# Kernel optimization log

Measured on AMD Instinct MI355X. Metric: run time of the kernel, lower is better.

Reference implementation:

```python
import jax, jax.numpy as jnp
import numpy as np
from itertools import combinations

S = 7                       # number of species (H,C,N,O,S,F,Cl)
RCR, RCA = 5.2, 3.5         # radial / angular cutoffs (Angstrom)
ETA_R, ETA_A, ZETA = 19.7, 12.5, 14.1
SHF_R = jnp.asarray(0.8 + 0.275 * np.arange(16), jnp.float32)        # 16 radial shifts
SHF_A = jnp.asarray(0.8 + 0.3375 * np.arange(8), jnp.float32)        # 8 angular radial shifts
SHF_Z = jnp.asarray((np.arange(4) + 0.5) * np.pi / 4, jnp.float32)   # 4 angle shifts
NPAIR = S * (S + 1) // 2    # 28 unordered species pairs
_t = np.zeros((S, S), np.int32); _c = 0
for _a in range(S):
    for _b in range(_a, S):
        _t[_a, _b] = _t[_b, _a] = _c; _c += 1
TRIU = jnp.asarray(_t)
AEV_DIM = S * 16 + NPAIR * 32   # 1008
M, H1, H2, H3 = 8, 256, 192, 160  # ensemble size and MLP widths


def _fc(d, rc):
    # torchani cutoff_cosine, masked for safety beyond rc
    return jnp.where(d < rc, 0.5 * jnp.cos(jnp.pi * d / rc) + 0.5, 0.0)


def compute_aev(sp, coords, atom_index12, triplet_index):
    # sp:[N] int, coords:[N,3], atom_index12:[2,P] half neighbor list,
    # triplet_index:[3,T] = (center, neighbor_j, neighbor_k)
    N = sp.shape[0]
    i, j = atom_index12[0], atom_index12[1]
    dvec = coords[j] - coords[i]
    dist = jnp.sqrt((dvec * dvec).sum(-1))
    fc = _fc(dist, RCR)
    rterm = 0.25 * jnp.exp(-ETA_R * (dist[:, None] - SHF_R) ** 2) * fc[:, None]  # [P,16]
    rad = jnp.zeros((N * S, 16), rterm.dtype)
    rad = rad.at[i * S + sp[j]].add(rterm).at[j * S + sp[i]].add(rterm)
    rad = rad.reshape(N, S * 16)

    c, a, b = triplet_index[0], triplet_index[1], triplet_index[2]
    v1 = coords[a] - coords[c]
    v2 = coords[b] - coords[c]
    d1 = jnp.sqrt((v1 * v1).sum(-1))
    d2 = jnp.sqrt((v2 * v2).sum(-1))
    cosang = 0.95 * (v1 * v2).sum(-1) / (d1 * d2)   # 0.95 numerical-safety factor as in torchani
    ang = jnp.arccos(cosang)
    fcj = _fc(d1, RCA) * _fc(d2, RCA)
    f1 = ((1.0 + jnp.cos(ang[:, None] - SHF_Z)) / 2.0) ** ZETA              # [T,4]
    f2 = jnp.exp(-ETA_A * ((d1 + d2)[:, None] / 2.0 - SHF_A) ** 2)          # [T,8]
    aterm = 2.0 * (f2[:, :, None] * f1[:, None, :]).reshape(-1, 32) * fcj[:, None]  # [T,32]
    pidx = TRIU[sp[a], sp[b]]
    angv = jnp.zeros((N * NPAIR, 32), aterm.dtype).at[c * NPAIR + pidx].add(aterm)
    return jnp.concatenate([rad, angv.reshape(N, NPAIR * 32)], axis=-1)     # [N,1008]


def _energy_and_force(species, coordinates, atom_index12, triplet_index, sgp,
                      W1, b1, W2, b2, W3, b3, W4, b4, sae):
    sp = species[0]
    sgpv = sgp[0]

    def total(coords):
        aev = compute_aev(sp, coords[0], atom_index12, triplet_index)       # [N,1008]
        h = jax.nn.celu(jnp.einsum('na,msab->msnb', aev, W1) + b1[:, :, None, :], alpha=0.1)
        h = jax.nn.celu(jnp.einsum('msnb,msbc->msnc', h, W2) + b2[:, :, None, :], alpha=0.1)
        h = jax.nn.celu(jnp.einsum('msnc,mscd->msnd', h, W3) + b3[:, :, None, :], alpha=0.1)
        e = jnp.einsum('msnd,msd->msn', h, W4) + b4[:, :, None]             # [M,S,N]
        onehot = (sgpv[None, :] == jnp.arange(S)[:, None]).astype(e.dtype)  # ghosts (-1) -> all-zero
        atomic = (e * onehot[None]).sum(1).mean(0)                           # [N] ensemble mean
        atomic = atomic + jnp.where(sgpv >= 0, sae[jnp.clip(sgpv, 0)], 0.0)  # energy shifter SAEs
        return atomic.sum()

    E = total(coordinates)
    force = -jax.grad(total)(coordinates)   # autograd force as in forward_total
    return E[None], force


def setup_inputs() -> dict:
    key = jax.random.key(0)
    n = 14; N = n ** 3   # 2744 atoms on a jittered cubic lattice (2.5 A spacing)
    ar = np.arange(n)
    gx, gy, gz = np.meshgrid(ar, ar, ar, indexing='ij')
    pos = np.stack([gx, gy, gz], -1).reshape(-1, 3)
    lid = lambda p: (p[:, 0] * n + p[:, 1]) * n + p[:, 2]
    # half neighbor list: all lattice offsets with |r| <= 5.2/2.5 lattice units
    half = [(1,0,0),(0,1,0),(0,0,1),(1,1,0),(1,-1,0),(1,0,1),(1,0,-1),(0,1,1),(0,1,-1),
            (1,1,1),(1,1,-1),(1,-1,1),(1,-1,-1),(2,0,0),(0,2,0),(0,0,2)]
    ei, ej = [], []
    for off in half:
        q = pos + np.array(off)
        m = ((q >= 0) & (q < n)).all(1)
        ei.append(lid(pos[m])); ej.append(lid(q[m]))
    atom_index12 = np.stack([np.concatenate(ei), np.concatenate(ej)]).astype(np.int32)
    # angular triplets: pairs of unit-offset neighbors (within Rca=3.5 A) per center
    unit = [(1,0,0),(-1,0,0),(0,1,0),(0,-1,0),(0,0,1),(0,0,-1)]
    nb = np.full((N, 6), -1, np.int64)
    for t, off in enumerate(unit):
        q = pos + np.array(off)
        m = ((q >= 0) & (q < n)).all(1)
        nb[lid(pos[m]), t] = lid(q[m])
    tc, tj, tk = [], [], []
    for a_, b_ in combinations(range(6), 2):
        m = (nb[:, a_] >= 0) & (nb[:, b_] >= 0)
        tc.append(np.nonzero(m)[0]); tj.append(nb[m, a_]); tk.append(nb[m, b_])
    triplet_index = np.stack([np.concatenate(tc), np.concatenate(tj), np.concatenate(tk)]).astype(np.int32)
    rng = np.random.default_rng(0)
    species = rng.integers(0, S, (1, N)).astype(np.int32)
    nghost = 250
    sgp = species.copy(); sgp[0, N - nghost:] = -1   # ghost atoms padded with -1
    coords = (pos.astype(np.float32) * 2.5 + 0.15 * rng.standard_normal((N, 3)).astype(np.float32))[None]
    ks = jax.random.split(key, 9)
    D = AEV_DIM
    W1 = jax.random.normal(ks[0], (M, S, D, H1), jnp.float32) * (D ** -0.5)
    b1 = 0.01 * jax.random.normal(ks[1], (M, S, H1), jnp.float32)
    W2 = jax.random.normal(ks[2], (M, S, H1, H2), jnp.float32) * (H1 ** -0.5)
    b2 = 0.01 * jax.random.normal(ks[3], (M, S, H2), jnp.float32)
    W3 = jax.random.normal(ks[4], (M, S, H2, H3), jnp.float32) * (H2 ** -0.5)
    b3 = 0.01 * jax.random.normal(ks[5], (M, S, H3), jnp.float32)
    W4 = jax.random.normal(ks[6], (M, S, H3), jnp.float32) * (H3 ** -0.5)
    b4 = 0.01 * jax.random.normal(ks[7], (M, S), jnp.float32)
    sae = jax.random.normal(ks[8], (S,), jnp.float32)
    return {
        'species': jnp.asarray(species), 'coordinates': jnp.asarray(coords),
        'atom_index12': jnp.asarray(atom_index12), 'triplet_index': jnp.asarray(triplet_index),
        'species_ghost_as_padding': jnp.asarray(sgp),
        'W1': W1, 'b1': b1, 'W2': W2, 'b2': b2, 'W3': W3, 'b3': b3, 'W4': W4, 'b4': b4, 'sae': sae,
    }


def reference(species, coordinates, atom_index12, triplet_index, species_ghost_as_padding,
              W1, b1, W2, b2, W3, b3, W4, b4, sae):
    return _energy_and_force(species, coordinates, atom_index12, triplet_index,
                             species_ghost_as_padding, W1, b1, W2, b2, W3, b3, W4, b4, sae)
```

## Files before the change

kernel.cpp:

```cpp
#include <hip/hip_runtime.h>
#include <math.h>

constexpr int SPEC = 7;
constexpr int DAEV = 1008;
constexpr int RADN = 112;
constexpr int H1W = 256, H2W = 192, H3W = 160;
constexpr int MENS = 8;
constexpr float ALPHA = 0.1f;
constexpr float RCR_ = 5.2f, RCA_ = 3.5f;
constexpr float ETAR = 19.7f, ETAA = 12.5f, ZETA_ = 14.1f;
constexpr float PIF = 3.14159265358979323846f;

enum { MODE_FWD = 0, MODE_BWD = 1, MODE_PLAIN = 2 };

typedef _Float16 f16x8 __attribute__((ext_vector_type(8)));
typedef float f32x4 __attribute__((ext_vector_type(4)));

__device__ inline f32x4 mfma16(f16x8 a, f16x8 b, f32x4 c) {
    return __builtin_amdgcn_mfma_f32_16x16x32_f16(a, b, c, 0, 0, 0);
}

__device__ inline void cvt_hilo(const float* xv, f16x8& h, f16x8& l) {
    #pragma unroll
    for (int e = 0; e < 8; ++e) {
        _Float16 hh = (_Float16)xv[e];
        h[e] = hh;
        l[e] = (_Float16)(xv[e] - (float)hh);
    }
}

__global__ __launch_bounds__(256) void build_lists_k(
    const int* __restrict__ sgp, int* __restrict__ counts,
    int* __restrict__ lists, int N)
{
    int n = blockIdx.x * blockDim.x + threadIdx.x;
    if (n >= N) return;
    int g = sgp[n];
    if (g >= 0) {
        int p = atomicAdd(&counts[g], 1);
        lists[g * N + p] = n;
    }
}

__global__ __launch_bounds__(256) void radial_fwd_k(
    const int* __restrict__ ai12, const int* __restrict__ spec,
    const float* __restrict__ coord, float* __restrict__ aev, int P)
{
    int p = blockIdx.x * blockDim.x + threadIdx.x;
    if (p >= P) return;
    int i = ai12[p], j = ai12[P + p];
    float dx = coord[3 * j + 0] - coord[3 * i + 0];
    float dy = coord[3 * j + 1] - coord[3 * i + 1];
    float dz = coord[3 * j + 2] - coord[3 * i + 2];
    float d = sqrtf(dx * dx + dy * dy + dz * dz);
    float fc = (d < RCR_) ? (0.5f * cosf(PIF * d / RCR_) + 0.5f) : 0.f;
    int spi = spec[i], spj = spec[j];
    float* bi = aev + (size_t)i * DAEV + spj * 16;
    float* bj = aev + (size_t)j * DAEV + spi * 16;
    #pragma unroll
    for (int k = 0; k < 16; ++k) {
        float sh = 0.8f + 0.275f * k;
        float t = d - sh;
        float v = 0.25f * expf(-ETAR * t * t) * fc;
        atomicAdd(bi + k, v);
        atomicAdd(bj + k, v);
    }
}

__global__ __launch_bounds__(256) void angular_fwd_k(
    const int* __restrict__ tri, const int* __restrict__ spec,
    const float* __restrict__ coord, float* __restrict__ aev, int T)
{
    int t = blockIdx.x * blockDim.x + threadIdx.x;
    if (t >= T) return;
    int c = tri[t], a = tri[T + t], b = tri[2 * T + t];
    float cx = coord[3 * c], cy = coord[3 * c + 1], cz = coord[3 * c + 2];
    float v1x = coord[3 * a] - cx, v1y = coord[3 * a + 1] - cy, v1z = coord[3 * a + 2] - cz;
    float v2x = coord[3 * b] - cx, v2y = coord[3 * b + 1] - cy, v2z = coord[3 * b + 2] - cz;
    float d1 = sqrtf(v1x * v1x + v1y * v1y + v1z * v1z);
    float d2 = sqrtf(v2x * v2x + v2y * v2y + v2z * v2z);
    float u = v1x * v2x + v1y * v2y + v1z * v2z;
    float ca = 0.95f * u / (d1 * d2);
    float sa = sqrtf(fmaxf(1.f - ca * ca, 0.f));
    float fc1 = (d1 < RCA_) ? (0.5f * cosf(PIF * d1 / RCA_) + 0.5f) : 0.f;
    float fc2 = (d2 < RCA_) ? (0.5f * cosf(PIF * d2 / RCA_) + 0.5f) : 0.f;
    float fcj = fc1 * fc2;
    float savg = 0.5f * (d1 + d2);
    int s1 = spec[a], s2 = spec[b];
    int lo = min(s1, s2), hi = max(s1, s2);
    int pidx = lo * SPEC - (lo * (lo - 1)) / 2 + (hi - lo);
    float* ob = aev + (size_t)c * DAEV + RADN + pidx * 32;
    const float CZ[4] = {0.92387953f, 0.38268343f, -0.38268343f, -0.92387953f};
    const float SZ[4] = {0.38268343f, 0.92387953f, 0.92387953f, 0.38268343f};
    float f1[4];
    #pragma unroll
    for (int zz = 0; zz < 4; ++zz) {
        float cd = ca * CZ[zz] + sa * SZ[zz];
        float base = fmaxf(0.5f * (1.f + cd), 0.f);
        f1[zz] = powf(base, ZETA_);
    }
    #pragma unroll
    for (int q = 0; q < 8; ++q) {
        float sh = 0.8f + 0.3375f * q;
        float tq = savg - sh;
        float f2 = expf(-ETAA * tq * tq);
        float b2 = 2.f * f2 * fcj;
        #pragma unroll
        for (int zz = 0; zz < 4; ++zz)
            atomicAdd(ob + q * 4 + zz, b2 * f1[zz]);
    }
}

template<int MODE, bool BT, bool MCONCAT>
__global__ __launch_bounds__(256) void mgemm_k(
    const float* __restrict__ A, const float* __restrict__ B,
    const float* __restrict__ bias, float* __restrict__ C,
    const int* __restrict__ lists, const int* __restrict__ counts,
    int N, int K, int H, int lda, int ldb, int ldc,
    size_t amOff, size_t bzOff, size_t cmOff)
{
    __shared__ f16x8 Ah[4][64];
    __shared__ f16x8 Al[4][64];
    __shared__ f16x8 Bh[4][128];
    __shared__ f16x8 Bl[4][128];
    __shared__ int atomsS[64];

    const int z = blockIdx.z;
    int m, sp_;
    if (MCONCAT) { sp_ = z; m = 0; } else { m = z / SPEC; sp_ = z - m * SPEC; }
    const int cnt = counts[sp_];
    const int row0 = blockIdx.y * 64;
    if (row0 >= cnt) return;
    const int col0 = blockIdx.x * 128;
    const int tid = threadIdx.x;

    const float* Ab = A + (size_t)m * amOff;
    const float* Bb = B + (size_t)z * bzOff;

    if (tid < 64) {
        int r = row0 + tid;
        atomsS[tid] = (r < cnt) ? lists[sp_ * N + r] : -1;
    }

    const int arow = tid >> 2, akq = tid & 3;
    const int bkg = tid >> 6;

    const int wid = tid >> 6, lane = tid & 63;
    const int wr = wid >> 1, wc = wid & 1;
    const int fr = lane & 15, q = lane >> 4;

    f32x4 acc[2][4];
    #pragma unroll
    for (int mi = 0; mi < 2; ++mi)
        #pragma unroll
        for (int ni = 0; ni < 4; ++ni)
            acc[mi][ni] = (f32x4){0.f, 0.f, 0.f, 0.f};

    for (int k0 = 0; k0 < K; k0 += 32) {
        __syncthreads();
        {
            int atom = atomsS[arow];
            int kbase = k0 + akq * 8;
            float xv[8];
            if (atom >= 0 && kbase < K) {
                const float* p;
                if (MCONCAT)
                    p = Ab + (size_t)(kbase >> 8) * ((size_t)N * H1W)
                           + (size_t)atom * H1W + (kbase & 255);
                else
                    p = Ab + (size_t)atom * lda + kbase;
                float4 u0 = *(const float4*)p;
                float4 u1 = *(const float4*)(p + 4);
                xv[0] = u0.x; xv[1] = u0.y; xv[2] = u0.z; xv[3] = u0.w;
                xv[4] = u1.x; xv[5] = u1.y; xv[6] = u1.z; xv[7] = u1.w;
            } else {
                #pragma unroll
                for (int e = 0; e < 8; ++e) xv[e] = 0.f;
            }
            f16x8 h, l;
            cvt_hilo(xv, h, l);
            int slot = arow ^ (akq << 2);
            Ah[akq][slot] = h;
            Al[akq][slot] = l;
        }
        {
            int kbase = k0 + bkg * 8;
            bool kok = (kbase < K);
            #pragma unroll
            for (int cc = 0; cc < 2; ++cc) {
                int c = (tid & 63) + cc * 64;
                int gc = col0 + c;
                float xv[8];
                if (kok && gc < H) {
                    if (BT) {
                        const float* p;
                        if (MCONCAT)
                            p = B + ((size_t)(kbase >> 8) * SPEC + sp_) * ((size_t)DAEV * H1W)
                                  + (size_t)gc * H1W + (kbase & 255);
                        else
                            p = Bb + (size_t)gc * ldb + kbase;
                        float4 u0 = *(const float4*)p;
                        float4 u1 = *(const float4*)(p + 4);
                        xv[0] = u0.x; xv[1] = u0.y; xv[2] = u0.z; xv[3] = u0.w;
                        xv[4] = u1.x; xv[5] = u1.y; xv[6] = u1.z; xv[7] = u1.w;
                    } else {
                        const float* p = Bb + (size_t)kbase * ldb + gc;
                        #pragma unroll
                        for (int j = 0; j < 8; ++j) xv[j] = p[(size_t)j * ldb];
                    }
                } else {
                    #pragma unroll
                    for (int e = 0; e < 8; ++e) xv[e] = 0.f;
                }
                f16x8 h, l;
                cvt_hilo(xv, h, l);
                Bh[bkg][c] = h;
                Bl[bkg][c] = l;
            }
        }
        __syncthreads();
        {
            f16x8 ah[2], av[2], bh[4], bv[4];
            #pragma unroll
            for (int mi = 0; mi < 2; ++mi) {
                int r = wr * 32 + mi * 16 + fr;
                int slot = r ^ (q << 2);
                ah[mi] = Ah[q][slot];
                av[mi] = Al[q][slot];
            }
            #pragma unroll
            for (int ni = 0; ni < 4; ++ni) {
                int c = wc * 64 + ni * 16 + fr;
                bh[ni] = Bh[q][c];
                bv[ni] = Bl[q][c];
            }
            #pragma unroll
            for (int mi = 0; mi < 2; ++mi)
                #pragma unroll
                for (int ni = 0; ni < 4; ++ni) {
                    acc[mi][ni] = mfma16(ah[mi], bv[ni], acc[mi][ni]);
                    acc[mi][ni] = mfma16(av[mi], bh[ni], acc[mi][ni]);
                    acc[mi][ni] = mfma16(ah[mi], bh[ni], acc[mi][ni]);
                }
        }
    }

    float* Cb = C + (size_t)m * cmOff;
    const float* brow = (MODE == MODE_FWD) ? (bias + (size_t)z * H) : nullptr;
    #pragma unroll
    for (int mi = 0; mi < 2; ++mi) {
        #pragma unroll
        for (int r = 0; r < 4; ++r) {
            int rl = wr * 32 + mi * 16 + q * 4 + r;
            int atom = atomsS[rl];
            if (atom < 0) continue;
            float* crow = Cb + (size_t)atom * ldc;
            #pragma unroll
            for (int ni = 0; ni < 4; ++ni) {
                int col = col0 + wc * 64 + ni * 16 + fr;
                if (col >= H) continue;
                float v = acc[mi][ni][r];
                if (MODE == MODE_FWD) {
                    v += brow[col];
                    v = (v > 0.f) ? v : ALPHA * expm1f(v * (1.f / ALPHA));
                } else if (MODE == MODE_BWD) {
                    float h = crow[col];
                    float D = (h > 0.f) ? 1.f : (h * (1.f / ALPHA) + 1.f);
                    v *= D;
                }
                crow[col] = v;
            }
        }
    }
}

__global__ __launch_bounds__(256) void l4_k(
    float* __restrict__ H3buf, const float* __restrict__ W4,
    const float* __restrict__ b4, const int* __restrict__ lists,
    const int* __restrict__ counts, float* __restrict__ Eout, int N)
{
    const int z = blockIdx.y;
    const int m = z / SPEC, s = z - m * SPEC;
    const int cnt = counts[s];
    const int sub = threadIdx.x >> 3;
    const int l8 = threadIdx.x & 7;
    const int row = blockIdx.x * 32 + sub;

    __shared__ float bsum;
    if (threadIdx.x == 0) bsum = 0.f;
    __syncthreads();

    if (row < cnt) {
        int atom = lists[s * N + row];
        float* hb = H3buf + ((size_t)m * N + atom) * H3W;
        const float* w4 = W4 + (size_t)z * H3W;
        float sum = 0.f;
        for (int k = l8; k < H3W; k += 8) {
            float h = hb[k];
            float w = w4[k];
            sum += h * w;
            float D = (h > 0.f) ? 1.f : (h * 10.f + 1.f);
            hb[k] = 0.125f * w * D;
        }
        sum += __shfl_xor(sum, 1);
        sum += __shfl_xor(sum, 2);
        sum += __shfl_xor(sum, 4);
        if (l8 == 0) atomicAdd(&bsum, sum + b4[z]);
    }
    __syncthreads();
    if (threadIdx.x == 0) atomicAdd(Eout, 0.125f * bsum);
}

__global__ __launch_bounds__(256) void radial_bwd_k(
    const int* __restrict__ ai12, const int* __restrict__ spec,
    const float* __restrict__ coord, const float* __restrict__ daev,
    float* __restrict__ grad, int P)
{
    int p = blockIdx.x * blockDim.x + threadIdx.x;
    if (p >= P) return;
    int i = ai12[p], j = ai12[P + p];
    float dx = coord[3 * j + 0] - coord[3 * i + 0];
    float dy = coord[3 * j + 1] - coord[3 * i + 1];
    float dz = coord[3 * j + 2] - coord[3 * i + 2];
    float d = sqrtf(dx * dx + dy * dy + dz * dz);
    float fc, dfc;
    if (d < RCR_) {
        float ph = PIF * d / RCR_;
        fc = 0.5f * cosf(ph) + 0.5f;
        dfc = -0.5f * sinf(ph) * (PIF / RCR_);
    } else { fc = 0.f; dfc = 0.f; }
    int spi = spec[i], spj = spec[j];
    const float* gi = daev + (size_t)i * DAEV + spj * 16;
    const float* gj = daev + (size_t)j * DAEV + spi * 16;
    float gs = 0.f;
    #pragma unroll
    for (int k = 0; k < 16; ++k) {
        float sh = 0.8f + 0.275f * k;
        float t = d - sh;
        float ex = expf(-ETAR * t * t);
        float g = gi[k] + gj[k];
        gs += g * 0.25f * ex * (dfc - 2.f * ETAR * t * fc);
    }
    float invd = 1.f / d;
    float gx = gs * dx * invd, gy = gs * dy * invd, gz = gs * dz * invd;
    atomicAdd(&grad[3 * j + 0], gx);  atomicAdd(&grad[3 * j + 1], gy);  atomicAdd(&grad[3 * j + 2], gz);
    atomicAdd(&grad[3 * i + 0], -gx); atomicAdd(&grad[3 * i + 1], -gy); atomicAdd(&grad[3 * i + 2], -gz);
}

__global__ __launch_bounds__(256) void angular_bwd_k(
    const int* __restrict__ tri, const int* __restrict__ spec,
    const float* __restrict__ coord, const float* __restrict__ daev,
    float* __restrict__ grad, int T)
{
    int t = blockIdx.x * blockDim.x + threadIdx.x;
    if (t >= T) return;
    int c = tri[t], a = tri[T + t], b = tri[2 * T + t];
    float cx = coord[3 * c], cy = coord[3 * c + 1], cz = coord[3 * c + 2];
    float v1x = coord[3 * a] - cx, v1y = coord[3 * a + 1] - cy, v1z = coord[3 * a + 2] - cz;
    float v2x = coord[3 * b] - cx, v2y = coord[3 * b + 1] - cy, v2z = coord[3 * b + 2] - cz;
    float d1 = sqrtf(v1x * v1x + v1y * v1y + v1z * v1z);
    float d2 = sqrtf(v2x * v2x + v2y * v2y + v2z * v2z);
    float u = v1x * v2x + v1y * v2y + v1z * v2z;
    float inv12 = 1.f / (d1 * d2);
    float ca = 0.95f * u * inv12;
    float sa = sqrtf(fmaxf(1.f - ca * ca, 1e-12f));
    float fc1, dfc1, fc2, dfc2;
    if (d1 < RCA_) {
        float ph = PIF * d1 / RCA_;
        fc1 = 0.5f * cosf(ph) + 0.5f;
        dfc1 = -0.5f * sinf(ph) * (PIF / RCA_);
    } else { fc1 = 0.f; dfc1 = 0.f; }
    if (d2 < RCA_) {
        float ph = PIF * d2 / RCA_;
        fc2 = 0.5f * cosf(ph) + 0.5f;
        dfc2 = -0.5f * sinf(ph) * (PIF / RCA_);
    } else { fc2 = 0.f; dfc2 = 0.f; }
    float fcj = fc1 * fc2;
    float savg = 0.5f * (d1 + d2);
    int s1 = spec[a], s2 = spec[b];
    int lo = min(s1, s2), hi = max(s1, s2);
    int pidx = lo * SPEC - (lo * (lo - 1)) / 2 + (hi - lo);
    const float* gb = daev + (size_t)c * DAEV + RADN + pidx * 32;
    const float CZ[4] = {0.92387953f, 0.38268343f, -0.38268343f, -0.92387953f};
    const float SZ[4] = {0.38268343f, 0.92387953f, 0.92387953f, 0.38268343f};
    float f1[4], df1[4];
    #pragma unroll
    for (int zz = 0; zz < 4; ++zz) {
        float cd = ca * CZ[zz] + sa * SZ[zz];
        float sd = sa * CZ[zz] - ca * SZ[zz];
        float base = fmaxf(0.5f * (1.f + cd), 0.f);
        float pm1 = powf(base, ZETA_ - 1.f);
        f1[zz] = pm1 * base;
        df1[zz] = ZETA_ * pm1 * (-0.5f * sd);
    }
    float A_ = 0.f, B_ = 0.f, Cc = 0.f;
    #pragma unroll
    for (int q = 0; q < 8; ++q) {
        float sh = 0.8f + 0.3375f * q;
        float tq = savg - sh;
        float f2 = expf(-ETAA * tq * tq);
        float df2 = -ETAA * tq * f2;
        #pragma unroll
        for (int zz = 0; zz < 4; ++zz) {
            float G2 = 2.f * gb[q * 4 + zz];
            A_ += G2 * f2 * df1[zz];
            B_ += G2 * df2 * f1[zz];
            Cc += G2 * f2 * f1[zz];
        }
    }
    A_ *= fcj; B_ *= fcj;
    float C1 = Cc * dfc1 * fc2;
    float C2 = Cc * fc1 * dfc2;
    float cA = -A_ / sa;
    float k12 = cA * 0.95f * inv12;
    float coef1 = (cA * (-ca) / d1 + B_ + C1) / d1;
    float coef2 = (cA * (-ca) / d2 + B_ + C2) / d2;
    float g1x = coef1 * v1x + k12 * v2x;
    float g1y = coef1 * v1y + k12 * v2y;
    float g1z = coef1 * v1z + k12 * v2z;
    float g2x = coef2 * v2x + k12 * v1x;
    float g2y = coef2 * v2y + k12 * v1y;
    float g2z = coef2 * v2z + k12 * v1z;
    atomicAdd(&grad[3 * a + 0], g1x); atomicAdd(&grad[3 * a + 1], g1y); atomicAdd(&grad[3 * a + 2], g1z);
    atomicAdd(&grad[3 * b + 0], g2x); atomicAdd(&grad[3 * b + 1], g2y); atomicAdd(&grad[3 * b + 2], g2z);
    atomicAdd(&grad[3 * c + 0], -(g1x + g2x));
    atomicAdd(&grad[3 * c + 1], -(g1y + g2y));
    atomicAdd(&grad[3 * c + 2], -(g1z + g2z));
}

__global__ __launch_bounds__(256) void finalize_k(
    const float* __restrict__ grad, const int* __restrict__ sgp,
    const float* __restrict__ sae, float* __restrict__ out, int N)
{
    int n = blockIdx.x * blockDim.x + threadIdx.x;
    __shared__ float bs;
    if (threadIdx.x == 0) bs = 0.f;
    __syncthreads();
    float v = 0.f;
    if (n < N) {
        out[1 + 3 * n + 0] = -grad[3 * n + 0];
        out[1 + 3 * n + 1] = -grad[3 * n + 1];
        out[1 + 3 * n + 2] = -grad[3 * n + 2];
        int g = sgp[n];
        if (g >= 0) v = sae[g];
    }
    atomicAdd(&bs, v);
    __syncthreads();
    if (threadIdx.x == 0) atomicAdd(out, bs);
}

extern "C" void kernel_launch(void* const* d_in, const int* in_sizes, int n_in,
                              void* d_out, int out_size, void* d_ws, size_t ws_size,
                              hipStream_t stream)
{
    (void)n_in; (void)out_size; (void)ws_size;
    const int* species = (const int*)d_in[0];
    const float* coords = (const float*)d_in[1];
    const int* ai12 = (const int*)d_in[2];
    const int* tri = (const int*)d_in[3];
    const int* sgp = (const int*)d_in[4];
    const float* W1 = (const float*)d_in[5];
    const float* b1 = (const float*)d_in[6];
    const float* W2 = (const float*)d_in[7];
    const float* b2 = (const float*)d_in[8];
    const float* W3 = (const float*)d_in[9];
    const float* b3 = (const float*)d_in[10];
    const float* W4 = (const float*)d_in[11];
    const float* b4 = (const float*)d_in[12];
    const float* sae = (const float*)d_in[13];
    float* out = (float*)d_out;

    const int N = in_sizes[0];
    const int P = in_sizes[2] / 2;
    const int T = in_sizes[3] / 3;

    float* ws = (float*)d_ws;
    size_t off = 0;
    float* aev  = ws + off; off += (size_t)N * DAEV;
    float* daev = ws + off; off += (size_t)N * DAEV;
    float* H1b  = ws + off; off += (size_t)MENS * N * H1W;
    float* H2b  = ws + off; off += (size_t)MENS * N * H2W;
    float* H3b  = ws + off; off += (size_t)MENS * N * H3W;
    float* grad = ws + off; off += (size_t)N * 3;
    int* counts = (int*)(ws + off); off += 8;
    int* lists  = (int*)(ws + off); off += (size_t)SPEC * N;

    hipMemsetAsync(aev, 0, (size_t)N * DAEV * 2 * sizeof(float), stream);
    hipMemsetAsync(grad, 0, (size_t)N * 3 * sizeof(float), stream);
    hipMemsetAsync(counts, 0, 8 * sizeof(int), stream);
    hipMemsetAsync(d_out, 0, sizeof(float), stream);

    build_lists_k<<<(N + 255) / 256, 256, 0, stream>>>(sgp, counts, lists, N);
    radial_fwd_k<<<(P + 255) / 256, 256, 0, stream>>>(ai12, species, coords, aev, P);
    angular_fwd_k<<<(T + 255) / 256, 256, 0, stream>>>(tri, species, coords, aev, T);

    const int rowTiles = (N + 63) / 64;
    mgemm_k<MODE_FWD, false, false><<<dim3(2, rowTiles, 56), 256, 0, stream>>>(
        aev, W1, b1, H1b, lists, counts, N, DAEV, H1W, DAEV, H1W, H1W,
        0, (size_t)DAEV * H1W, (size_t)N * H1W);
    mgemm_k<MODE_FWD, false, false><<<dim3(2, rowTiles, 56), 256, 0, stream>>>(
        H1b, W2, b2, H2b, lists, counts, N, H1W, H2W, H1W, H2W, H2W,
        (size_t)N * H1W, (size_t)H1W * H2W, (size_t)N * H2W);
    mgemm_k<MODE_FWD, false, false><<<dim3(2, rowTiles, 56), 256, 0, stream>>>(
        H2b, W3, b3, H3b, lists, counts, N, H2W, H3W, H2W, H3W, H3W,
        (size_t)N * H2W, (size_t)H2W * H3W, (size_t)N * H3W);
    l4_k<<<dim3((N + 31) / 32, 56), 256, 0, stream>>>(H3b, W4, b4, lists, counts, out, N);
    mgemm_k<MODE_BWD, true, false><<<dim3(2, rowTiles, 56), 256, 0, stream>>>(
        H3b, W3, nullptr, H2b, lists, counts, N, H3W, H2W, H3W, H3W, H2W,
        (size_t)N * H3W, (size_t)H2W * H3W, (size_t)N * H2W);
    mgemm_k<MODE_BWD, true, false><<<dim3(2, rowTiles, 56), 256, 0, stream>>>(
        H2b, W2, nullptr, H1b, lists, counts, N, H2W, H1W, H2W, H2W, H1W,
        (size_t)N * H2W, (size_t)H1W * H2W, (size_t)N * H1W);
    mgemm_k<MODE_PLAIN, true, true><<<dim3(8, rowTiles, 7), 256, 0, stream>>>(
        H1b, W1, nullptr, daev, lists, counts, N, MENS * H1W, DAEV, 0, 0, DAEV,
        0, 0, 0);

    radial_bwd_k<<<(P + 255) / 256, 256, 0, stream>>>(ai12, species, coords, daev, grad, P);
    angular_bwd_k<<<(T + 255) / 256, 256, 0, stream>>>(tri, species, coords, daev, grad, T);
    finalize_k<<<(N + 255) / 256, 256, 0, stream>>>(grad, sgp, sae, out, N);
}
```

Baseline: 732.5 us.

## Store activations as fp16 hi/lo pairs, pre-split weights, and prefetch GEMM tiles

Intermediate activations H1-H3 are now stored as split fp16 hi/lo pairs instead of fp32, and W2/W3 are converted once per launch into fp16 hi/lo layouts (transposed for the forward pass) by a new wconv kernel. The GEMM kernel no longer converts these operands per tile, and it prefetches the next K-tile into registers while the current one is computed. The aev buffer is reused for daev to cut workspace. This aims to reduce conversion work, strided weight loads and memory traffic, at the cost of extra weight-conversion launches and slightly changed rounding of stored activations.

```diff
diff --git a/kernel.cpp b/kernel.cpp
--- a/kernel.cpp
+++ b/kernel.cpp
@@ -16,16 +16,17 @@
 typedef _Float16 f16x8 __attribute__((ext_vector_type(8)));
 typedef float f32x4 __attribute__((ext_vector_type(4)));
 
-__device__ inline f32x4 mfma16(f16x8 a, f16x8 b, f32x4 c) {
+__device__ __forceinline__ f32x4 mfma16(f16x8 a, f16x8 b, f32x4 c) {
     return __builtin_amdgcn_mfma_f32_16x16x32_f16(a, b, c, 0, 0, 0);
 }
 
-__device__ inline void cvt_hilo(const float* xv, f16x8& h, f16x8& l) {
+__device__ __forceinline__ void cvt8(float4 u0, float4 u1, f16x8& h, f16x8& l) {
+    float x[8] = {u0.x, u0.y, u0.z, u0.w, u1.x, u1.y, u1.z, u1.w};
     #pragma unroll
     for (int e = 0; e < 8; ++e) {
-        _Float16 hh = (_Float16)xv[e];
+        _Float16 hh = (_Float16)x[e];
         h[e] = hh;
-        l[e] = (_Float16)(xv[e] - (float)hh);
+        l[e] = (_Float16)(x[e] - (float)hh);
     }
 }
 
@@ -111,19 +112,64 @@
     }
 }
 
-template<int MODE, bool BT, bool MCONCAT>
+template<bool DO_O, bool DO_T>
+__global__ __launch_bounds__(256) void wconv_k(
+    const float* __restrict__ W,
+    _Float16* __restrict__ oH, _Float16* __restrict__ oL,
+    _Float16* __restrict__ tH, _Float16* __restrict__ tL,
+    int K, int C, int ldt)
+{
+    __shared__ _Float16 sh[64][65];
+    __shared__ _Float16 sl[64][65];
+    const int z = blockIdx.z;
+    const int k0 = blockIdx.y * 64, c0 = blockIdx.x * 64;
+    const float* Wz = W + (size_t)z * K * C;
+    const int c = threadIdx.x & 63, qr = threadIdx.x >> 6;
+    #pragma unroll
+    for (int rr = 0; rr < 16; ++rr) {
+        int r = qr * 16 + rr;
+        int k = k0 + r, cc = c0 + c;
+        float v = (k < K && cc < C) ? Wz[(size_t)k * C + cc] : 0.f;
+        _Float16 h = (_Float16)v;
+        _Float16 l = (_Float16)(v - (float)h);
+        if (DO_O && k < K && cc < C) {
+            oH[(size_t)z * K * C + (size_t)k * C + cc] = h;
+            oL[(size_t)z * K * C + (size_t)k * C + cc] = l;
+        }
+        if (DO_T) { sh[r][c] = h; sl[r][c] = l; }
+    }
+    if (DO_T) {
+        __syncthreads();
+        #pragma unroll
+        for (int rr = 0; rr < 16; ++rr) {
+            int r = qr * 16 + rr;
+            int crow = c0 + r, kcol = k0 + c;
+            if (crow < C && kcol < ldt) {
+                tH[(size_t)z * C * ldt + (size_t)crow * ldt + kcol] = sh[c][r];
+                tL[(size_t)z * C * ldt + (size_t)crow * ldt + kcol] = sl[c][r];
+            }
+        }
+    }
+}
+
+template<int MODE, int ASRC, int BSRC, bool MCONCAT>
 __global__ __launch_bounds__(256) void mgemm_k(
-    const float* __restrict__ A, const float* __restrict__ B,
-    const float* __restrict__ bias, float* __restrict__ C,
+    const void* __restrict__ Ah_, const void* __restrict__ Al_,
+    const void* __restrict__ Bh_, const void* __restrict__ Bl_,
+    const float* __restrict__ bias, float* __restrict__ cF,
+    _Float16* __restrict__ cH, _Float16* __restrict__ cL,
     const int* __restrict__ lists, const int* __restrict__ counts,
-    int N, int K, int H, int lda, int ldb, int ldc,
-    size_t amOff, size_t bzOff, size_t cmOff)
-{
-    __shared__ f16x8 Ah[4][64];
-    __shared__ f16x8 Al[4][64];
-    __shared__ f16x8 Bh[4][128];
-    __shared__ f16x8 Bl[4][128];
+    int N, int K, int KA, int H, int lda, int ldb, int ldc,
+    size_t aStrM, size_t bStrZ, size_t cStrM)
+{
+    __shared__ f16x8 AhS[4][64];
+    __shared__ f16x8 AlS[4][64];
+    __shared__ float4 BU4[1056];
     __shared__ int atomsS[64];
+
+    f16x8* BhS = (f16x8*)BU4;
+    f16x8* BlS = BhS + 512;
+    float* Bf = (float*)BU4;
 
     const int z = blockIdx.z;
     int m, sp_;
@@ -133,20 +179,110 @@
     if (row0 >= cnt) return;
     const int col0 = blockIdx.x * 128;
     const int tid = threadIdx.x;
-
-    const float* Ab = A + (size_t)m * amOff;
-    const float* Bb = B + (size_t)z * bzOff;
-
-    if (tid < 64) {
-        int r = row0 + tid;
-        atomsS[tid] = (r < cnt) ? lists[sp_ * N + r] : -1;
-    }
-
-    const int arow = tid >> 2, akq = tid & 3;
-    const int bkg = tid >> 6;
-
-    const int wid = tid >> 6, lane = tid & 63;
-    const int wr = wid >> 1, wc = wid & 1;
+    const int w = tid >> 6, lane = tid & 63;
+
+    const int rA = min(row0 + lane, cnt - 1);
+    const int atomA = lists[sp_ * N + rA];
+    if (tid < 64) atomsS[tid] = atomA;
+
+    const int bc0 = min(col0 + lane, H - 1);
+    const int bc1 = min(col0 + 64 + lane, H - 1);
+
+    f16x8 rAh, rAl;
+    float4 rAf0, rAf1;
+    f16x8 rBh0, rBl0, rBh1, rBl1;
+    float4 rBf[4];
+
+    auto LOAD = [&](int k0s) {
+        int kk = k0s + w * 8;
+        if constexpr (ASRC == 0) {
+            const _Float16* ah = (const _Float16*)Ah_;
+            const _Float16* al = (const _Float16*)Al_;
+            size_t ao;
+            if constexpr (MCONCAT) {
+                int mm = kk >> 8, kr = kk & 255;
+                ao = ((size_t)mm * N + atomA) * (size_t)lda + kr;
+            } else {
+                ao = (size_t)m * aStrM + (size_t)atomA * lda + kk;
+            }
+            rAh = *(const f16x8*)(ah + ao);
+            rAl = *(const f16x8*)(al + ao);
+        } else {
+            const float* af = (const float*)Ah_;
+            if (kk < KA) {
+                const float* p = af + (size_t)atomA * lda + kk;
+                rAf0 = *(const float4*)p;
+                rAf1 = *(const float4*)(p + 4);
+            } else {
+                rAf0 = make_float4(0.f, 0.f, 0.f, 0.f);
+                rAf1 = rAf0;
+            }
+        }
+        if constexpr (BSRC == 0) {
+            const _Float16* bh = (const _Float16*)Bh_;
+            const _Float16* bl = (const _Float16*)Bl_;
+            size_t b0 = (size_t)z * bStrZ + (size_t)bc0 * ldb + kk;
+            size_t b1 = (size_t)z * bStrZ + (size_t)bc1 * ldb + kk;
+            rBh0 = *(const f16x8*)(bh + b0);
+            rBh1 = *(const f16x8*)(bh + b1);
+            rBl0 = *(const f16x8*)(bl + b0);
+            rBl1 = *(const f16x8*)(bl + b1);
+        } else if constexpr (BSRC == 1) {
+            const float* bf = (const float*)Bh_;
+            int mm = kk >> 8, kr = kk & 255;
+            size_t b0 = ((size_t)(mm * SPEC + sp_) * DAEV + bc0) * (size_t)ldb + kr;
+            size_t b1 = ((size_t)(mm * SPEC + sp_) * DAEV + bc1) * (size_t)ldb + kr;
+            rBf[0] = *(const float4*)(bf + b0);
+            rBf[1] = *(const float4*)(bf + b0 + 4);
+            rBf[2] = *(const float4*)(bf + b1);
+            rBf[3] = *(const float4*)(bf + b1 + 4);
+        } else {
+            const float* bf = (const float*)Bh_ + (size_t)z * bStrZ;
+            #pragma unroll
+            for (int p = 0; p < 4; ++p) {
+                int kl = p * 8 + (tid >> 5);
+                int kg = k0s + kl;
+                if (kg < KA)
+                    rBf[p] = *(const float4*)(bf + (size_t)kg * ldb + col0 + (tid & 31) * 4);
+                else
+                    rBf[p] = make_float4(0.f, 0.f, 0.f, 0.f);
+            }
+        }
+    };
+
+    auto WRITE = [&]() {
+        if constexpr (ASRC == 0) {
+            AhS[w][lane] = rAh;
+            AlS[w][lane] = rAl;
+        } else {
+            f16x8 h, l;
+            cvt8(rAf0, rAf1, h, l);
+            AhS[w][lane] = h;
+            AlS[w][lane] = l;
+        }
+        if constexpr (BSRC == 0) {
+            BhS[w * 128 + lane] = rBh0;
+            BhS[w * 128 + 64 + lane] = rBh1;
+            BlS[w * 128 + lane] = rBl0;
+            BlS[w * 128 + 64 + lane] = rBl1;
+        } else if constexpr (BSRC == 1) {
+            f16x8 h, l;
+            cvt8(rBf[0], rBf[1], h, l);
+            BhS[w * 128 + lane] = h;
+            BlS[w * 128 + lane] = l;
+            cvt8(rBf[2], rBf[3], h, l);
+            BhS[w * 128 + 64 + lane] = h;
+            BlS[w * 128 + 64 + lane] = l;
+        } else {
+            #pragma unroll
+            for (int p = 0; p < 4; ++p) {
+                int kl = p * 8 + (tid >> 5);
+                *(float4*)(Bf + kl * 132 + (tid & 31) * 4) = rBf[p];
+            }
+        }
+    };
+
+    const int wr = w >> 1, wc = w & 1;
     const int fr = lane & 15, q = lane >> 4;
 
     f32x4 acc[2][4];
@@ -156,128 +292,93 @@
         for (int ni = 0; ni < 4; ++ni)
             acc[mi][ni] = (f32x4){0.f, 0.f, 0.f, 0.f};
 
-    for (int k0 = 0; k0 < K; k0 += 32) {
+    const int nt = K / 32;
+    LOAD(0);
+
+    for (int t = 0; t < nt; ++t) {
         __syncthreads();
-        {
-            int atom = atomsS[arow];
-            int kbase = k0 + akq * 8;
-            float xv[8];
-            if (atom >= 0 && kbase < K) {
-                const float* p;
-                if (MCONCAT)
-                    p = Ab + (size_t)(kbase >> 8) * ((size_t)N * H1W)
-                           + (size_t)atom * H1W + (kbase & 255);
-                else
-                    p = Ab + (size_t)atom * lda + kbase;
-                float4 u0 = *(const float4*)p;
-                float4 u1 = *(const float4*)(p + 4);
-                xv[0] = u0.x; xv[1] = u0.y; xv[2] = u0.z; xv[3] = u0.w;
-                xv[4] = u1.x; xv[5] = u1.y; xv[6] = u1.z; xv[7] = u1.w;
-            } else {
-                #pragma unroll
-                for (int e = 0; e < 8; ++e) xv[e] = 0.f;
-            }
-            f16x8 h, l;
-            cvt_hilo(xv, h, l);
-            int slot = arow ^ (akq << 2);
-            Ah[akq][slot] = h;
-            Al[akq][slot] = l;
-        }
-        {
-            int kbase = k0 + bkg * 8;
-            bool kok = (kbase < K);
-            #pragma unroll
-            for (int cc = 0; cc < 2; ++cc) {
-                int c = (tid & 63) + cc * 64;
-                int gc = col0 + c;
-                float xv[8];
-                if (kok && gc < H) {
-                    if (BT) {
-                        const float* p;
-                        if (MCONCAT)
-                            p = B + ((size_t)(kbase >> 8) * SPEC + sp_) * ((size_t)DAEV * H1W)
-                                  + (size_t)gc * H1W + (kbase & 255);
-                        else
-                            p = Bb + (size_t)gc * ldb + kbase;
-                        float4 u0 = *(const float4*)p;
-                        float4 u1 = *(const float4*)(p + 4);
-                        xv[0] = u0.x; xv[1] = u0.y; xv[2] = u0.z; xv[3] = u0.w;
-                        xv[4] = u1.x; xv[5] = u1.y; xv[6] = u1.z; xv[7] = u1.w;
-                    } else {
-                        const float* p = Bb + (size_t)kbase * ldb + gc;
-                        #pragma unroll
-                        for (int j = 0; j < 8; ++j) xv[j] = p[(size_t)j * ldb];
-                    }
-                } else {
-                    #pragma unroll
-                    for (int e = 0; e < 8; ++e) xv[e] = 0.f;
-                }
-                f16x8 h, l;
-                cvt_hilo(xv, h, l);
-                Bh[bkg][c] = h;
-                Bl[bkg][c] = l;
-            }
-        }
+        WRITE();
         __syncthreads();
-        {
-            f16x8 ah[2], av[2], bh[4], bv[4];
-            #pragma unroll
-            for (int mi = 0; mi < 2; ++mi) {
-                int r = wr * 32 + mi * 16 + fr;
-                int slot = r ^ (q << 2);
-                ah[mi] = Ah[q][slot];
-                av[mi] = Al[q][slot];
-            }
+        if (t + 1 < nt) LOAD((t + 1) * 32);
+
+        f16x8 fah[2], fal[2], fbh[4], fbl[4];
+        #pragma unroll
+        for (int mi = 0; mi < 2; ++mi) {
+            int r = wr * 32 + mi * 16 + fr;
+            fah[mi] = AhS[q][r];
+            fal[mi] = AlS[q][r];
+        }
+        if constexpr (BSRC <= 1) {
             #pragma unroll
             for (int ni = 0; ni < 4; ++ni) {
                 int c = wc * 64 + ni * 16 + fr;
-                bh[ni] = Bh[q][c];
-                bv[ni] = Bl[q][c];
-            }
+                fbh[ni] = BhS[q * 128 + c];
+                fbl[ni] = BlS[q * 128 + c];
+            }
+        } else {
             #pragma unroll
-            for (int mi = 0; mi < 2; ++mi)
+            for (int ni = 0; ni < 4; ++ni) {
+                int c = wc * 64 + ni * 16 + fr;
                 #pragma unroll
-                for (int ni = 0; ni < 4; ++ni) {
-                    acc[mi][ni] = mfma16(ah[mi], bv[ni], acc[mi][ni]);
-                    acc[mi][ni] = mfma16(av[mi], bh[ni], acc[mi][ni]);
-                    acc[mi][ni] = mfma16(ah[mi], bh[ni], acc[mi][ni]);
+                for (int j = 0; j < 8; ++j) {
+                    float v = Bf[(q * 8 + j) * 132 + c];
+                    _Float16 hh = (_Float16)v;
+                    fbh[ni][j] = hh;
+                    fbl[ni][j] = (_Float16)(v - (float)hh);
                 }
-        }
-    }
-
-    float* Cb = C + (size_t)m * cmOff;
+            }
+        }
+        #pragma unroll
+        for (int mi = 0; mi < 2; ++mi)
+            #pragma unroll
+            for (int ni = 0; ni < 4; ++ni) {
+                acc[mi][ni] = mfma16(fah[mi], fbl[ni], acc[mi][ni]);
+                acc[mi][ni] = mfma16(fal[mi], fbh[ni], acc[mi][ni]);
+                acc[mi][ni] = mfma16(fah[mi], fbh[ni], acc[mi][ni]);
+            }
+    }
+
     const float* brow = (MODE == MODE_FWD) ? (bias + (size_t)z * H) : nullptr;
     #pragma unroll
     for (int mi = 0; mi < 2; ++mi) {
         #pragma unroll
         for (int r = 0; r < 4; ++r) {
             int rl = wr * 32 + mi * 16 + q * 4 + r;
+            if (row0 + rl >= cnt) continue;
             int atom = atomsS[rl];
-            if (atom < 0) continue;
-            float* crow = Cb + (size_t)atom * ldc;
+            size_t rowoff = (size_t)m * cStrM + (size_t)atom * ldc;
             #pragma unroll
             for (int ni = 0; ni < 4; ++ni) {
                 int col = col0 + wc * 64 + ni * 16 + fr;
                 if (col >= H) continue;
                 float v = acc[mi][ni][r];
+                size_t idx = rowoff + col;
                 if (MODE == MODE_FWD) {
                     v += brow[col];
                     v = (v > 0.f) ? v : ALPHA * expm1f(v * (1.f / ALPHA));
+                    _Float16 hh = (_Float16)v;
+                    cH[idx] = hh;
+                    cL[idx] = (_Float16)(v - (float)hh);
                 } else if (MODE == MODE_BWD) {
-                    float h = crow[col];
-                    float D = (h > 0.f) ? 1.f : (h * (1.f / ALPHA) + 1.f);
+                    float hprev = (float)cH[idx] + (float)cL[idx];
+                    float D = (hprev > 0.f) ? 1.f : (hprev * (1.f / ALPHA) + 1.f);
                     v *= D;
+                    _Float16 hh = (_Float16)v;
+                    cH[idx] = hh;
+                    cL[idx] = (_Float16)(v - (float)hh);
+                } else {
+                    cF[idx] = v;
                 }
-                crow[col] = v;
             }
         }
     }
 }
 
 __global__ __launch_bounds__(256) void l4_k(
-    float* __restrict__ H3buf, const float* __restrict__ W4,
-    const float* __restrict__ b4, const int* __restrict__ lists,
-    const int* __restrict__ counts, float* __restrict__ Eout, int N)
+    _Float16* __restrict__ h3H, _Float16* __restrict__ h3L,
+    const float* __restrict__ W4, const float* __restrict__ b4,
+    const int* __restrict__ lists, const int* __restrict__ counts,
+    float* __restrict__ Eout, int N)
 {
     const int z = blockIdx.y;
     const int m = z / SPEC, s = z - m * SPEC;
@@ -292,15 +393,18 @@
 
     if (row < cnt) {
         int atom = lists[s * N + row];
-        float* hb = H3buf + ((size_t)m * N + atom) * H3W;
+        size_t base = ((size_t)m * N + atom) * H3W;
         const float* w4 = W4 + (size_t)z * H3W;
         float sum = 0.f;
         for (int k = l8; k < H3W; k += 8) {
-            float h = hb[k];
-            float w = w4[k];
-            sum += h * w;
+            float h = (float)h3H[base + k] + (float)h3L[base + k];
+            float wv = w4[k];
+            sum += h * wv;
             float D = (h > 0.f) ? 1.f : (h * 10.f + 1.f);
-            hb[k] = 0.125f * w * D;
+            float g = 0.125f * wv * D;
+            _Float16 gh = (_Float16)g;
+            h3H[base + k] = gh;
+            h3L[base + k] = (_Float16)(g - (float)gh);
         }
         sum += __shfl_xor(sum, 1);
         sum += __shfl_xor(sum, 2);
@@ -473,19 +577,27 @@
     const int N = in_sizes[0];
     const int P = in_sizes[2] / 2;
     const int T = in_sizes[3] / 3;
+    const size_t NM = (size_t)MENS * N;
 
     float* ws = (float*)d_ws;
     size_t off = 0;
-    float* aev  = ws + off; off += (size_t)N * DAEV;
-    float* daev = ws + off; off += (size_t)N * DAEV;
-    float* H1b  = ws + off; off += (size_t)MENS * N * H1W;
-    float* H2b  = ws + off; off += (size_t)MENS * N * H2W;
-    float* H3b  = ws + off; off += (size_t)MENS * N * H3W;
-    float* grad = ws + off; off += (size_t)N * 3;
-    int* counts = (int*)(ws + off); off += 8;
-    int* lists  = (int*)(ws + off); off += (size_t)SPEC * N;
-
-    hipMemsetAsync(aev, 0, (size_t)N * DAEV * 2 * sizeof(float), stream);
+    auto alloc = [&](size_t nf) { float* p = ws + off; off += nf; return p; };
+
+    float* aev = alloc((size_t)N * DAEV);
+    _Float16* H1h = (_Float16*)alloc(NM * 128);
+    _Float16* H1l = (_Float16*)alloc(NM * 128);
+    _Float16* H2h = (_Float16*)alloc(NM * 96);
+    _Float16* H2l = (_Float16*)alloc(NM * 96);
+    _Float16* H3h = (_Float16*)alloc(NM * 80);
+    _Float16* H3l = (_Float16*)alloc(NM * 80);
+    _Float16* Wh = (_Float16*)alloc((size_t)56 * 96 * 256);
+    _Float16* Wl = (_Float16*)alloc((size_t)56 * 96 * 256);
+    float* grad = alloc((size_t)N * 3);
+    int* counts = (int*)alloc(8);
+    int* lists = (int*)alloc((size_t)SPEC * N);
+    float* daev = aev;
+
+    hipMemsetAsync(aev, 0, (size_t)N * DAEV * sizeof(float), stream);
     hipMemsetAsync(grad, 0, (size_t)N * 3 * sizeof(float), stream);
     hipMemsetAsync(counts, 0, 8 * sizeof(int), stream);
     hipMemsetAsync(d_out, 0, sizeof(float), stream);
@@ -494,25 +606,49 @@
     radial_fwd_k<<<(P + 255) / 256, 256, 0, stream>>>(ai12, species, coords, aev, P);
     angular_fwd_k<<<(T + 255) / 256, 256, 0, stream>>>(tri, species, coords, aev, T);
 
-    const int rowTiles = (N + 63) / 64;
-    mgemm_k<MODE_FWD, false, false><<<dim3(2, rowTiles, 56), 256, 0, stream>>>(
-        aev, W1, b1, H1b, lists, counts, N, DAEV, H1W, DAEV, H1W, H1W,
-        0, (size_t)DAEV * H1W, (size_t)N * H1W);
-    mgemm_k<MODE_FWD, false, false><<<dim3(2, rowTiles, 56), 256, 0, stream>>>(
-        H1b, W2, b2, H2b, lists, counts, N, H1W, H2W, H1W, H2W, H2W,
-        (size_t)N * H1W, (size_t)H1W * H2W, (size_t)N * H2W);
-    mgemm_k<MODE_FWD, false, false><<<dim3(2, rowTiles, 56), 256, 0, stream>>>(
-        H2b, W3, b3, H3b, lists, counts, N, H2W, H3W, H2W, H3W, H3W,
-        (size_t)N * H2W, (size_t)H2W * H3W, (size_t)N * H3W);
-    l4_k<<<dim3((N + 31) / 32, 56), 256, 0, stream>>>(H3b, W4, b4, lists, counts, out, N);
-    mgemm_k<MODE_BWD, true, false><<<dim3(2, rowTiles, 56), 256, 0, stream>>>(
-        H3b, W3, nullptr, H2b, lists, counts, N, H3W, H2W, H3W, H3W, H2W,
-        (size_t)N * H3W, (size_t)H2W * H3W, (size_t)N * H2W);
-    mgemm_k<MODE_BWD, true, false><<<dim3(2, rowTiles, 56), 256, 0, stream>>>(
-        H2b, W2, nullptr, H1b, lists, counts, N, H2W, H1W, H2W, H2W, H1W,
-        (size_t)N * H2W, (size_t)H1W * H2W, (size_t)N * H1W);
-    mgemm_k<MODE_PLAIN, true, true><<<dim3(8, rowTiles, 7), 256, 0, stream>>>(
-        H1b, W1, nullptr, daev, lists, counts, N, MENS * H1W, DAEV, 0, 0, DAEV,
+    const int rt = (N + 63) / 64;
+
+    mgemm_k<MODE_FWD, 1, 2, false><<<dim3(2, rt, 56), 256, 0, stream>>>(
+        aev, nullptr, W1, nullptr, b1, nullptr, H1h, H1l,
+        lists, counts, N, 1024, 1008, 256, 1008, 256, 256,
+        0, (size_t)1008 * 256, (size_t)N * 256);
+
+    wconv_k<false, true><<<dim3(3, 4, 56), 256, 0, stream>>>(
+        W2, nullptr, nullptr, Wh, Wl, 256, 192, 256);
+    mgemm_k<MODE_FWD, 0, 0, false><<<dim3(2, rt, 56), 256, 0, stream>>>(
+        H1h, H1l, Wh, Wl, b2, nullptr, H2h, H2l,
+        lists, counts, N, 256, 256, 192, 256, 256, 192,
+        (size_t)N * 256, (size_t)192 * 256, (size_t)N * 192);
+
+    wconv_k<false, true><<<dim3(3, 3, 56), 256, 0, stream>>>(
+        W3, nullptr, nullptr, Wh, Wl, 192, 160, 192);
+    mgemm_k<MODE_FWD, 0, 0, false><<<dim3(2, rt, 56), 256, 0, stream>>>(
+        H2h, H2l, Wh, Wl, b3, nullptr, H3h, H3l,
+        lists, counts, N, 192, 192, 160, 192, 192, 160,
+        (size_t)N * 192, (size_t)160 * 192, (size_t)N * 160);
+
+    l4_k<<<dim3((N + 31) / 32, 56), 256, 0, stream>>>(
+        H3h, H3l, W4, b4, lists, counts, out, N);
+
+    hipMemsetAsync(daev, 0, (size_t)N * DAEV * sizeof(float), stream);
+
+    wconv_k<true, false><<<dim3(3, 3, 56), 256, 0, stream>>>(
+        W3, Wh, Wl, nullptr, nullptr, 192, 160, 0);
+    mgemm_k<MODE_BWD, 0, 0, false><<<dim3(2, rt, 56), 256, 0, stream>>>(
+        H3h, H3l, Wh, Wl, nullptr, nullptr, H2h, H2l,
+        lists, counts, N, 160, 160, 192, 160, 160, 192,
+        (size_t)N * 160, (size_t)192 * 160, (size_t)N * 192);
+
+    wconv_k<true, false><<<dim3(3, 4, 56), 256, 0, stream>>>(
+        W2, Wh, Wl, nullptr, nullptr, 256, 192, 0);
+    mgemm_k<MODE_BWD, 0, 0, false><<<dim3(2, rt, 56), 256, 0, stream>>>(
+        H2h, H2l, Wh, Wl, nullptr, nullptr, H1h, H1l,
+        lists, counts, N, 192, 192, 256, 192, 192, 256,
+        (size_t)N * 192, (size_t)256 * 192, (size_t)N * 256);
+
+    mgemm_k<MODE_PLAIN, 0, 1, true><<<dim3(8, rt, 7), 256, 0, stream>>>(
+        H1h, H1l, W1, nullptr, nullptr, daev, nullptr, nullptr,
+        lists, counts, N, 2048, 2048, 1008, 256, 256, 1008,
         0, 0, 0);
 
     radial_bwd_k<<<(P + 255) / 256, 256, 0, stream>>>(ai12, species, coords, daev, grad, P);
```

After: 862.7 us. 1.18x slower.
